# Kernel optimization log

Hardware: AMD Instinct MI355X
Metric: run time of the kernel (lower is better)

The kernel has to match this reference:

```python
import jax, jax.numpy as jnp
import numpy as np

H = 64    # hidden_size
IN = 7    # input_size
Q = 3     # output_size = len(quantiles)
T = 288   # target_len


def _lstm_cell(x, h, c, W_ih, W_hh, b_ih, b_hh):
    # PyTorch gate order: i, f, g, o. W_ih: [4H, in], W_hh: [4H, H]
    gates = x @ W_ih.T + h @ W_hh.T + (b_ih + b_hh)  # [B, 4H]
    i, f, g, o = jnp.split(gates, 4, axis=-1)
    i = jax.nn.sigmoid(i)
    f = jax.nn.sigmoid(f)
    g = jnp.tanh(g)
    o = jax.nn.sigmoid(o)
    c_new = f * c + i * g
    h_new = o * jnp.tanh(c_new)
    return h_new, c_new


def setup_inputs() -> dict:
    key = jax.random.key(0)
    ks = jax.random.split(key, 12)
    B, S = 2048, 512
    scale = 1.0 / np.sqrt(H)  # matches PyTorch uniform(-1/sqrt(H), 1/sqrt(H)) magnitude
    u = lambda k, shape: jax.random.uniform(k, shape, jnp.float32, -scale, scale)
    return {
        "x": jax.random.normal(ks[0], (B, S, IN), dtype=jnp.float32),
        "enc_W_ih": u(ks[1], (4 * H, IN)),
        "enc_W_hh": u(ks[2], (4 * H, H)),
        "enc_b_ih": u(ks[3], (4 * H,)),
        "enc_b_hh": u(ks[4], (4 * H,)),
        "dec_W_ih": u(ks[5], (4 * H, Q)),
        "dec_W_hh": u(ks[6], (4 * H, H)),
        "dec_b_ih": u(ks[7], (4 * H,)),
        "dec_b_hh": u(ks[8], (4 * H,)),
        "out_W": u(ks[9], (Q, H)),
        "out_b": u(ks[10], (Q,)),
    }


def reference(x, enc_W_ih, enc_W_hh, enc_b_ih, enc_b_hh,
              dec_W_ih, dec_W_hh, dec_b_ih, dec_b_hh, out_W, out_b):
    B = x.shape[0]
    # ---- Encoder LSTM over the full sequence; keep only final (h, c) ----
    h0 = jnp.zeros((B, H), dtype=x.dtype)
    c0 = jnp.zeros((B, H), dtype=x.dtype)

    def enc_step(carry, x_t):
        h, c = carry
        h, c = _lstm_cell(x_t, h, c, enc_W_ih, enc_W_hh, enc_b_ih, enc_b_hh)
        return (h, c), None

    (h_enc, c_enc), _ = jax.lax.scan(enc_step, (h0, c0), jnp.swapaxes(x, 0, 1))

    # ---- Decoder: each of the T steps restarts from the FIXED encoder state
    # (the original discards the decoder's returned state), feeding back the
    # previous output. Dropout is identity at inference. ----
    def dec_step(dec_in, _):
        h1, _c1 = _lstm_cell(dec_in, h_enc, c_enc,
                             dec_W_ih, dec_W_hh, dec_b_ih, dec_b_hh)
        out = h1 @ out_W.T + out_b  # [B, Q]
        return out, out

    dec_in0 = jnp.zeros((B, Q), dtype=x.dtype)
    _, outputs = jax.lax.scan(dec_step, dec_in0, None, length=T)  # [T, B, Q]
    return jnp.transpose(outputs, (1, 0, 2))  # [B, T, Q]; out_dict[q] = out[:, :, i]
```

## Files before the change

### kernel.cpp

```cpp
#include <hip/hip_runtime.h>

#define HDIM  64
#define INDIM 7
#define QDIM  3
#define TDEC  288
#define SEQ   512
#define NBT   8
#define CHUNK 32
#define HPAD  68
#define GPAD  264
#define HBST  80
#define PXU   264

typedef __attribute__((ext_vector_type(8))) short bf16x8;
typedef __attribute__((ext_vector_type(4))) float f32x4;

__device__ __forceinline__ float fast_rcp(float x) { return __builtin_amdgcn_rcpf(x); }
__device__ __forceinline__ float sigm(float x) { return fast_rcp(1.0f + __expf(-x)); }
__device__ __forceinline__ float tanh_f(float x) {
    float e = __expf(2.0f * x);
    return fmaf(-2.0f, fast_rcp(1.0f + e), 1.0f);
}
__device__ __forceinline__ short f2bf(float f) {
    union { float f; unsigned u; } v; v.f = f;
    unsigned r = (v.u + 0x7fffu + ((v.u >> 16) & 1u)) >> 16;
    return (short)r;
}
__device__ __forceinline__ float bf2f(short s) {
    union { unsigned u; float f; } v; v.u = ((unsigned)(unsigned short)s) << 16;
    return v.f;
}

__global__ __launch_bounds__(512, 2)
void enc_dec_kernel(const float* __restrict__ x,
                    const float* __restrict__ eWih, const float* __restrict__ eWhh,
                    const float* __restrict__ ebih, const float* __restrict__ ebhh,
                    const float* __restrict__ dWih, const float* __restrict__ dWhh,
                    const float* __restrict__ dbih, const float* __restrict__ dbhh,
                    const float* __restrict__ oW,   const float* __restrict__ obv,
                    float* __restrict__ out)
{
    __shared__ __align__(16) short lds_hh[2][NBT][HBST];
    __shared__ __align__(16) short lds_xbh[2][CHUNK][NBT][8];
    __shared__ __align__(16) short lds_xbl[2][CHUNK][NBT][8];
    __shared__ __align__(16) short lds_xzero[8];
    __shared__ __align__(16) float lds_px[2][4][NBT][PXU];
    __shared__ __align__(16) float lds_hf[NBT][HPAD];
    __shared__ __align__(16) float lds_cf[NBT][HPAD];
    __shared__ __align__(16) float lds_g[NBT][GPAD];

    const int tid  = threadIdx.x;
    const int lane = tid & 63;
    const int wid  = tid >> 6;
    const int b0   = blockIdx.x * NBT;

    const int m    = lane & 15;
    const int g16  = lane >> 4;
    const int b_act = lane & 7;
    const int tsel  = (lane >> 3) & 1;
    const int u_act = wid * 8 + tsel * 4 + g16;

    bf16x8 a_hi[2][2], a_lo[2][2];
#pragma unroll
    for (int tt = 0; tt < 2; ++tt) {
        const int t = 2 * wid + tt;
        const int row = (m & 3) * 64 + 4 * t + (m >> 2);
#pragma unroll
        for (int kt = 0; kt < 2; ++kt) {
            const float* p = eWhh + (size_t)row * HDIM + kt * 32 + g16 * 8;
            f32x4 v0 = *(const f32x4*)p;
            f32x4 v1 = *(const f32x4*)(p + 4);
#pragma unroll
            for (int e = 0; e < 4; ++e) {
                short hi = f2bf(v0[e]);
                a_hi[tt][kt][e] = hi;
                a_lo[tt][kt][e] = f2bf(v0[e] - bf2f(hi));
            }
#pragma unroll
            for (int e = 0; e < 4; ++e) {
                short hi = f2bf(v1[e]);
                a_hi[tt][kt][4 + e] = hi;
                a_lo[tt][kt][4 + e] = f2bf(v1[e] - bf2f(hi));
            }
        }
    }

    bf16x8 axh[2], axl[2];
#pragma unroll
    for (int tt = 0; tt < 2; ++tt) {
        const int t = 2 * wid + tt;
        const int row = (m & 3) * 64 + 4 * t + (m >> 2);
        if (g16 == 0) {
#pragma unroll
            for (int e = 0; e < 8; ++e) {
                float v = (e < 7) ? eWih[row * INDIM + e] : (ebih[row] + ebhh[row]);
                short hi = f2bf(v);
                axh[tt][e] = hi;
                axl[tt][e] = f2bf(v - bf2f(hi));
            }
        } else {
#pragma unroll
            for (int e = 0; e < 8; ++e) { axh[tt][e] = 0; axl[tt][e] = 0; }
        }
    }

    lds_hh[1][wid][lane] = 0;
    if (tid < 8) lds_xzero[tid] = 0;
    float c_reg = 0.0f;

    auto load_x_chunk = [&](int xbuf, int s0) {
        for (int i = tid; i < NBT * CHUNK * 8; i += 512) {
            int b = i >> 8;
            int r = i & 255;
            int ss = r >> 3;
            int k = r & 7;
            float v = (k < 7) ? x[((size_t)(b0 + b) * SEQ + (s0 + ss)) * INDIM + k] : 1.0f;
            short hi = f2bf(v);
            lds_xbh[xbuf][ss][b][k] = hi;
            lds_xbl[xbuf][ss][b][k] = f2bf(v - bf2f(hi));
        }
    };

    auto compute_xw = [&](int j2) {
        const int sbase = 4 * j2;
        const int xbuf  = (sbase >> 5) & 1;
        const int sr0   = sbase & 31;
        const int col16 = lane & 15;
        const int pxb   = j2 & 1;
        bf16x8 bxh[2], bxl[2];
#pragma unroll
        for (int n = 0; n < 2; ++n) {
            const int srow = sr0 + 2 * n + (col16 >> 3);
            const short* ph = (g16 == 0) ? &lds_xbh[xbuf][srow][lane & 7][0] : &lds_xzero[0];
            const short* pl = (g16 == 0) ? &lds_xbl[xbuf][srow][lane & 7][0] : &lds_xzero[0];
            bxh[n] = *(const bf16x8*)ph;
            bxl[n] = *(const bf16x8*)pl;
        }
#pragma unroll
        for (int tt = 0; tt < 2; ++tt) {
#pragma unroll
            for (int n = 0; n < 2; ++n) {
                f32x4 p = {0, 0, 0, 0};
                p = __builtin_amdgcn_mfma_f32_16x16x32_bf16(axh[tt], bxh[n], p, 0, 0, 0);
                p = __builtin_amdgcn_mfma_f32_16x16x32_bf16(axl[tt], bxh[n], p, 0, 0, 0);
                p = __builtin_amdgcn_mfma_f32_16x16x32_bf16(axh[tt], bxl[n], p, 0, 0, 0);
                const int sl = 2 * n + (col16 >> 3);
                const int u  = 4 * (2 * wid + tt) + (lane >> 4);
                *(f32x4*)&lds_px[pxb][sl][lane & 7][u * 4] = p;
            }
        }
    };

    load_x_chunk(0, 0);
    __syncthreads();
    compute_xw(0);
    __syncthreads();

    for (int s = 0; s < SEQ; ++s) {
        const int cs  = s & (CHUNK - 1);
        const int rb  = (s & 1) ^ 1;
        const int wb  = s & 1;

        f32x4 px4 = *(const f32x4*)&lds_px[(s >> 2) & 1][s & 3][b_act][u_act * 4];

        bf16x8 bh[2];
#pragma unroll
        for (int kt = 0; kt < 2; ++kt)
            bh[kt] = *(const bf16x8*)&lds_hh[rb][b_act][kt * 32 + g16 * 8];

        f32x4 acc0 = {0, 0, 0, 0}, acc1 = {0, 0, 0, 0};
#pragma unroll
        for (int kt = 0; kt < 2; ++kt) {
            acc0 = __builtin_amdgcn_mfma_f32_16x16x32_bf16(a_hi[0][kt], bh[kt], acc0, 0, 0, 0);
            acc1 = __builtin_amdgcn_mfma_f32_16x16x32_bf16(a_hi[1][kt], bh[kt], acc1, 0, 0, 0);
            acc0 = __builtin_amdgcn_mfma_f32_16x16x32_bf16(a_lo[0][kt], bh[kt], acc0, 0, 0, 0);
            acc1 = __builtin_amdgcn_mfma_f32_16x16x32_bf16(a_lo[1][kt], bh[kt], acc1, 0, 0, 0);
        }

        float pre[4];
#pragma unroll
        for (int g = 0; g < 4; ++g) pre[g] = tsel ? acc1[g] : acc0[g];

        {
#pragma unroll
            for (int g = 0; g < 4; ++g) pre[g] += px4[g];
            float ig = sigm(pre[0]), fg = sigm(pre[1]), gg = tanh_f(pre[2]), og = sigm(pre[3]);
            c_reg = fg * c_reg + ig * gg;
            float h = og * tanh_f(c_reg);
            lds_hh[wb][b_act][u_act] = f2bf(h);
            if (s + 1 == SEQ) {
                lds_hf[b_act][u_act] = h;
                lds_cf[b_act][u_act] = c_reg;
            }
        }

        if ((s & 3) == 0 && s + 4 < SEQ) compute_xw((s >> 2) + 1);

        if (cs == 0 && s + CHUNK < SEQ) {
            load_x_chunk(((s >> 5) & 1) ^ 1, s + CHUNK);
        }
        __syncthreads();
    }

    {
        const int row = tid & 255;
        const int gh  = tid >> 8;
        float4 dwhh[16];
#pragma unroll
        for (int m4 = 0; m4 < 16; ++m4)
            dwhh[m4] = *reinterpret_cast<const float4*>(&dWhh[row * HDIM + m4 * 4]);
        const float dbias = dbih[row] + dbhh[row];

        float accd[4];
#pragma unroll
        for (int b = 0; b < 4; ++b) accd[b] = dbias;
#pragma unroll
        for (int m4 = 0; m4 < 16; ++m4) {
            const float4 w = dwhh[m4];
            float4 hv[4];
#pragma unroll
            for (int b = 0; b < 4; ++b)
                hv[b] = *reinterpret_cast<const float4*>(&lds_hf[gh * 4 + b][m4 * 4]);
#pragma unroll
            for (int b = 0; b < 4; ++b) accd[b] = fmaf(hv[b].x, w.x, accd[b]);
#pragma unroll
            for (int b = 0; b < 4; ++b) accd[b] = fmaf(hv[b].y, w.y, accd[b]);
#pragma unroll
            for (int b = 0; b < 4; ++b) accd[b] = fmaf(hv[b].z, w.z, accd[b]);
#pragma unroll
            for (int b = 0; b < 4; ++b) accd[b] = fmaf(hv[b].w, w.w, accd[b]);
        }
#pragma unroll
        for (int b = 0; b < 4; ++b) lds_g[gh * 4 + b][row] = accd[b];
    }
    __syncthreads();

    {
        const int b = wid, j = lane;
        const float c_e = lds_cf[b][j];
        const float gb0 = lds_g[b][j];
        const float gb1 = lds_g[b][HDIM + j];
        const float gb2 = lds_g[b][2 * HDIM + j];
        const float gb3 = lds_g[b][3 * HDIM + j];

        const float w00 = dWih[(0 * HDIM + j) * QDIM + 0], w01 = dWih[(0 * HDIM + j) * QDIM + 1], w02 = dWih[(0 * HDIM + j) * QDIM + 2];
        const float w10 = dWih[(1 * HDIM + j) * QDIM + 0], w11 = dWih[(1 * HDIM + j) * QDIM + 1], w12 = dWih[(1 * HDIM + j) * QDIM + 2];
        const float w20 = dWih[(2 * HDIM + j) * QDIM + 0], w21 = dWih[(2 * HDIM + j) * QDIM + 1], w22 = dWih[(2 * HDIM + j) * QDIM + 2];
        const float w30 = dWih[(3 * HDIM + j) * QDIM + 0], w31 = dWih[(3 * HDIM + j) * QDIM + 1], w32 = dWih[(3 * HDIM + j) * QDIM + 2];
        const float ow0 = oW[0 * HDIM + j], ow1 = oW[1 * HDIM + j], ow2 = oW[2 * HDIM + j];
        const float ob0 = obv[0], ob1 = obv[1], ob2 = obv[2];

        float y0 = 0.0f, y1 = 0.0f, y2 = 0.0f;
        float* outp = out + (size_t)(b0 + b) * TDEC * QDIM;

        for (int t = 0; t < TDEC; ++t) {
            float g0 = gb0 + y0 * w00 + y1 * w01 + y2 * w02;
            float g1 = gb1 + y0 * w10 + y1 * w11 + y2 * w12;
            float g2 = gb2 + y0 * w20 + y1 * w21 + y2 * w22;
            float g3 = gb3 + y0 * w30 + y1 * w31 + y2 * w32;
            float ig = sigm(g0), fg = sigm(g1), gg = tanh_f(g2), og = sigm(g3);
            float c = fg * c_e + ig * gg;
            float h = og * tanh_f(c);
            float r0 = h * ow0, r1 = h * ow1, r2 = h * ow2;
#pragma unroll
            for (int d = 1; d < 64; d <<= 1) {
                r0 += __shfl_xor(r0, d);
                r1 += __shfl_xor(r1, d);
                r2 += __shfl_xor(r2, d);
            }
            y0 = r0 + ob0;
            y1 = r1 + ob1;
            y2 = r2 + ob2;
            if (j < QDIM) outp[t * QDIM + j] = (j == 0) ? y0 : (j == 1) ? y1 : y2;
        }
    }
}

extern "C" void kernel_launch(void* const* d_in, const int* in_sizes, int n_in,
                              void* d_out, int out_size, void* d_ws, size_t ws_size,
                              hipStream_t stream) {
    (void)in_sizes; (void)n_in; (void)d_ws; (void)ws_size; (void)out_size;
    const float* x    = (const float*)d_in[0];
    const float* eWih = (const float*)d_in[1];
    const float* eWhh = (const float*)d_in[2];
    const float* ebih = (const float*)d_in[3];
    const float* ebhh = (const float*)d_in[4];
    const float* dWih = (const float*)d_in[5];
    const float* dWhh = (const float*)d_in[6];
    const float* dbih = (const float*)d_in[7];
    const float* dbhh = (const float*)d_in[8];
    const float* oW   = (const float*)d_in[9];
    const float* obv  = (const float*)d_in[10];
    float* out = (float*)d_out;

    const int B = 2048;
    dim3 grid(B / NBT), block(512);
    enc_dec_kernel<<<grid, block, 0, stream>>>(x, eWih, eWhh, ebih, ebhh,
                                               dWih, dWhh, dbih, dbhh, oW, obv, out);
}
```

Measured before the change: 405.0 us.

## Halve batch tile per block to four rows with 256-thread blocks

Measured after the change: 444.3 us. 1.1x slower.

```diff
diff --git a/kernel.cpp b/kernel.cpp
--- a/kernel.cpp
+++ b/kernel.cpp
@@ -5,7 +5,7 @@
 #define QDIM  3
 #define TDEC  288
 #define SEQ   512
-#define NBT   8
+#define NBT   4
 #define CHUNK 32
 #define HPAD  68
 #define GPAD  264
@@ -31,7 +31,7 @@
     return v.f;
 }
 
-__global__ __launch_bounds__(512, 2)
+__global__ __launch_bounds__(256, 2)
 void enc_dec_kernel(const float* __restrict__ x,
                     const float* __restrict__ eWih, const float* __restrict__ eWhh,
                     const float* __restrict__ ebih, const float* __restrict__ ebhh,
@@ -56,14 +56,14 @@
 
     const int m    = lane & 15;
     const int g16  = lane >> 4;
-    const int b_act = lane & 7;
-    const int tsel  = (lane >> 3) & 1;
-    const int u_act = wid * 8 + tsel * 4 + g16;
-
-    bf16x8 a_hi[2][2], a_lo[2][2];
-#pragma unroll
-    for (int tt = 0; tt < 2; ++tt) {
-        const int t = 2 * wid + tt;
+    const int b_act = lane & 3;
+    const int tsel  = (lane >> 2) & 3;
+    const int u_act = wid * 16 + tsel * 4 + g16;
+
+    bf16x8 a_hi[4][2], a_lo[4][2];
+#pragma unroll
+    for (int tt = 0; tt < 4; ++tt) {
+        const int t = 4 * wid + tt;
         const int row = (m & 3) * 64 + 4 * t + (m >> 2);
 #pragma unroll
         for (int kt = 0; kt < 2; ++kt) {
@@ -85,10 +85,10 @@
         }
     }
 
-    bf16x8 axh[2], axl[2];
-#pragma unroll
-    for (int tt = 0; tt < 2; ++tt) {
-        const int t = 2 * wid + tt;
+    bf16x8 axh[4], axl[4];
+#pragma unroll
+    for (int tt = 0; tt < 4; ++tt) {
+        const int t = 4 * wid + tt;
         const int row = (m & 3) * 64 + 4 * t + (m >> 2);
         if (g16 == 0) {
 #pragma unroll
@@ -109,7 +109,7 @@
     float c_reg = 0.0f;
 
     auto load_x_chunk = [&](int xbuf, int s0) {
-        for (int i = tid; i < NBT * CHUNK * 8; i += 512) {
+        for (int i = tid; i < NBT * CHUNK * 8; i += 256) {
             int b = i >> 8;
             int r = i & 255;
             int ss = r >> 3;
@@ -125,29 +125,24 @@
         const int sbase = 4 * j2;
         const int xbuf  = (sbase >> 5) & 1;
         const int sr0   = sbase & 31;
-        const int col16 = lane & 15;
         const int pxb   = j2 & 1;
-        bf16x8 bxh[2], bxl[2];
-#pragma unroll
-        for (int n = 0; n < 2; ++n) {
-            const int srow = sr0 + 2 * n + (col16 >> 3);
-            const short* ph = (g16 == 0) ? &lds_xbh[xbuf][srow][lane & 7][0] : &lds_xzero[0];
-            const short* pl = (g16 == 0) ? &lds_xbl[xbuf][srow][lane & 7][0] : &lds_xzero[0];
-            bxh[n] = *(const bf16x8*)ph;
-            bxl[n] = *(const bf16x8*)pl;
-        }
-#pragma unroll
-        for (int tt = 0; tt < 2; ++tt) {
-#pragma unroll
-            for (int n = 0; n < 2; ++n) {
-                f32x4 p = {0, 0, 0, 0};
-                p = __builtin_amdgcn_mfma_f32_16x16x32_bf16(axh[tt], bxh[n], p, 0, 0, 0);
-                p = __builtin_amdgcn_mfma_f32_16x16x32_bf16(axl[tt], bxh[n], p, 0, 0, 0);
-                p = __builtin_amdgcn_mfma_f32_16x16x32_bf16(axh[tt], bxl[n], p, 0, 0, 0);
-                const int sl = 2 * n + (col16 >> 3);
-                const int u  = 4 * (2 * wid + tt) + (lane >> 4);
-                *(f32x4*)&lds_px[pxb][sl][lane & 7][u * 4] = p;
-            }
+        const int bb    = lane & 3;
+        const int slot  = (lane >> 2) & 3;
+        bf16x8 bxh, bxl;
+        {
+            const short* ph = (g16 == 0) ? &lds_xbh[xbuf][sr0 + slot][bb][0] : &lds_xzero[0];
+            const short* pl = (g16 == 0) ? &lds_xbl[xbuf][sr0 + slot][bb][0] : &lds_xzero[0];
+            bxh = *(const bf16x8*)ph;
+            bxl = *(const bf16x8*)pl;
+        }
+#pragma unroll
+        for (int tt = 0; tt < 4; ++tt) {
+            f32x4 p = {0, 0, 0, 0};
+            p = __builtin_amdgcn_mfma_f32_16x16x32_bf16(axh[tt], bxh, p, 0, 0, 0);
+            p = __builtin_amdgcn_mfma_f32_16x16x32_bf16(axl[tt], bxh, p, 0, 0, 0);
+            p = __builtin_amdgcn_mfma_f32_16x16x32_bf16(axh[tt], bxl, p, 0, 0, 0);
+            const int u = 4 * (4 * wid + tt) + (lane >> 4);
+            *(f32x4*)&lds_px[pxb][slot][bb][u * 4] = p;
         }
     };
 
@@ -168,18 +163,24 @@
         for (int kt = 0; kt < 2; ++kt)
             bh[kt] = *(const bf16x8*)&lds_hh[rb][b_act][kt * 32 + g16 * 8];
 
-        f32x4 acc0 = {0, 0, 0, 0}, acc1 = {0, 0, 0, 0};
+        f32x4 acc[4] = {{0,0,0,0},{0,0,0,0},{0,0,0,0},{0,0,0,0}};
 #pragma unroll
         for (int kt = 0; kt < 2; ++kt) {
-            acc0 = __builtin_amdgcn_mfma_f32_16x16x32_bf16(a_hi[0][kt], bh[kt], acc0, 0, 0, 0);
-            acc1 = __builtin_amdgcn_mfma_f32_16x16x32_bf16(a_hi[1][kt], bh[kt], acc1, 0, 0, 0);
-            acc0 = __builtin_amdgcn_mfma_f32_16x16x32_bf16(a_lo[0][kt], bh[kt], acc0, 0, 0, 0);
-            acc1 = __builtin_amdgcn_mfma_f32_16x16x32_bf16(a_lo[1][kt], bh[kt], acc1, 0, 0, 0);
+#pragma unroll
+            for (int tt = 0; tt < 4; ++tt)
+                acc[tt] = __builtin_amdgcn_mfma_f32_16x16x32_bf16(a_hi[tt][kt], bh[kt], acc[tt], 0, 0, 0);
+#pragma unroll
+            for (int tt = 0; tt < 4; ++tt)
+                acc[tt] = __builtin_amdgcn_mfma_f32_16x16x32_bf16(a_lo[tt][kt], bh[kt], acc[tt], 0, 0, 0);
         }
 
         float pre[4];
 #pragma unroll
-        for (int g = 0; g < 4; ++g) pre[g] = tsel ? acc1[g] : acc0[g];
+        for (int g = 0; g < 4; ++g) {
+            float s01 = (tsel & 1) ? acc[1][g] : acc[0][g];
+            float s23 = (tsel & 1) ? acc[3][g] : acc[2][g];
+            pre[g] = (tsel & 2) ? s23 : s01;
+        }
 
         {
 #pragma unroll
@@ -203,35 +204,34 @@
     }
 
     {
-        const int row = tid & 255;
-        const int gh  = tid >> 8;
+        const int row = wid * HDIM + lane;
         float4 dwhh[16];
 #pragma unroll
         for (int m4 = 0; m4 < 16; ++m4)
             dwhh[m4] = *reinterpret_cast<const float4*>(&dWhh[row * HDIM + m4 * 4]);
         const float dbias = dbih[row] + dbhh[row];
 
-        float accd[4];
-#pragma unroll
-        for (int b = 0; b < 4; ++b) accd[b] = dbias;
+        float accd[NBT];
+#pragma unroll
+        for (int b = 0; b < NBT; ++b) accd[b] = dbias;
 #pragma unroll
         for (int m4 = 0; m4 < 16; ++m4) {
             const float4 w = dwhh[m4];
-            float4 hv[4];
-#pragma unroll
-            for (int b = 0; b < 4; ++b)
-                hv[b] = *reinterpret_cast<const float4*>(&lds_hf[gh * 4 + b][m4 * 4]);
-#pragma unroll
-            for (int b = 0; b < 4; ++b) accd[b] = fmaf(hv[b].x, w.x, accd[b]);
-#pragma unroll
-            for (int b = 0; b < 4; ++b) accd[b] = fmaf(hv[b].y, w.y, accd[b]);
-#pragma unroll
-            for (int b = 0; b < 4; ++b) accd[b] = fmaf(hv[b].z, w.z, accd[b]);
-#pragma unroll
-            for (int b = 0; b < 4; ++b) accd[b] = fmaf(hv[b].w, w.w, accd[b]);
-        }
-#pragma unroll
-        for (int b = 0; b < 4; ++b) lds_g[gh * 4 + b][row] = accd[b];
+            float4 hv[NBT];
+#pragma unroll
+            for (int b = 0; b < NBT; ++b)
+                hv[b] = *reinterpret_cast<const float4*>(&lds_hf[b][m4 * 4]);
+#pragma unroll
+            for (int b = 0; b < NBT; ++b) accd[b] = fmaf(hv[b].x, w.x, accd[b]);
+#pragma unroll
+            for (int b = 0; b < NBT; ++b) accd[b] = fmaf(hv[b].y, w.y, accd[b]);
+#pragma unroll
+            for (int b = 0; b < NBT; ++b) accd[b] = fmaf(hv[b].z, w.z, accd[b]);
+#pragma unroll
+            for (int b = 0; b < NBT; ++b) accd[b] = fmaf(hv[b].w, w.w, accd[b]);
+        }
+#pragma unroll
+        for (int b = 0; b < NBT; ++b) lds_g[b][row] = accd[b];
     }
     __syncthreads();
 
@@ -294,7 +294,7 @@
     float* out = (float*)d_out;
 
     const int B = 2048;
-    dim3 grid(B / NBT), block(512);
+    dim3 grid(B / NBT), block(256);
     enc_dec_kernel<<<grid, block, 0, stream>>>(x, eWih, eWhh, ebih, ebhh,
                                                dWih, dWhh, dbih, dbhh, oW, obv, out);
 }
```

## Drop bf16 hi/lo split for encoder W_hh and use DPP wave reductions

Applied to the files above, without the earlier changes.

Result: faster. 356.0 us, median of 2 (-12.1%).

```diff
diff --git a/kernel.cpp b/kernel.cpp
--- a/kernel.cpp
+++ b/kernel.cpp
@@ -29,6 +29,21 @@
 __device__ __forceinline__ float bf2f(short s) {
     union { unsigned u; float f; } v; v.u = ((unsigned)(unsigned short)s) << 16;
     return v.f;
+}
+
+template<int CTRL>
+__device__ __forceinline__ float dpp_add(float v) {
+    int p = __builtin_amdgcn_update_dpp(0, __float_as_int(v), CTRL, 0xF, 0xF, true);
+    return v + __int_as_float(p);
+}
+__device__ __forceinline__ float wave_sum(float v) {
+    v = dpp_add<0xB1>(v);
+    v = dpp_add<0x4E>(v);
+    v = dpp_add<0x124>(v);
+    v = dpp_add<0x128>(v);
+    v += __shfl_xor(v, 16);
+    v += __shfl_xor(v, 32);
+    return v;
 }
 
 __global__ __launch_bounds__(512, 2)
@@ -60,7 +75,7 @@
     const int tsel  = (lane >> 3) & 1;
     const int u_act = wid * 8 + tsel * 4 + g16;
 
-    bf16x8 a_hi[2][2], a_lo[2][2];
+    bf16x8 a_h[2][2];
 #pragma unroll
     for (int tt = 0; tt < 2; ++tt) {
         const int t = 2 * wid + tt;
@@ -71,17 +86,9 @@
             f32x4 v0 = *(const f32x4*)p;
             f32x4 v1 = *(const f32x4*)(p + 4);
 #pragma unroll
-            for (int e = 0; e < 4; ++e) {
-                short hi = f2bf(v0[e]);
-                a_hi[tt][kt][e] = hi;
-                a_lo[tt][kt][e] = f2bf(v0[e] - bf2f(hi));
-            }
-#pragma unroll
-            for (int e = 0; e < 4; ++e) {
-                short hi = f2bf(v1[e]);
-                a_hi[tt][kt][4 + e] = hi;
-                a_lo[tt][kt][4 + e] = f2bf(v1[e] - bf2f(hi));
-            }
+            for (int e = 0; e < 4; ++e) a_h[tt][kt][e]     = f2bf(v0[e]);
+#pragma unroll
+            for (int e = 0; e < 4; ++e) a_h[tt][kt][4 + e] = f2bf(v1[e]);
         }
     }
 
@@ -171,10 +178,8 @@
         f32x4 acc0 = {0, 0, 0, 0}, acc1 = {0, 0, 0, 0};
 #pragma unroll
         for (int kt = 0; kt < 2; ++kt) {
-            acc0 = __builtin_amdgcn_mfma_f32_16x16x32_bf16(a_hi[0][kt], bh[kt], acc0, 0, 0, 0);
-            acc1 = __builtin_amdgcn_mfma_f32_16x16x32_bf16(a_hi[1][kt], bh[kt], acc1, 0, 0, 0);
-            acc0 = __builtin_amdgcn_mfma_f32_16x16x32_bf16(a_lo[0][kt], bh[kt], acc0, 0, 0, 0);
-            acc1 = __builtin_amdgcn_mfma_f32_16x16x32_bf16(a_lo[1][kt], bh[kt], acc1, 0, 0, 0);
+            acc0 = __builtin_amdgcn_mfma_f32_16x16x32_bf16(a_h[0][kt], bh[kt], acc0, 0, 0, 0);
+            acc1 = __builtin_amdgcn_mfma_f32_16x16x32_bf16(a_h[1][kt], bh[kt], acc1, 0, 0, 0);
         }
 
         float pre[4];
@@ -261,13 +266,9 @@
             float ig = sigm(g0), fg = sigm(g1), gg = tanh_f(g2), og = sigm(g3);
             float c = fg * c_e + ig * gg;
             float h = og * tanh_f(c);
-            float r0 = h * ow0, r1 = h * ow1, r2 = h * ow2;
-#pragma unroll
-            for (int d = 1; d < 64; d <<= 1) {
-                r0 += __shfl_xor(r0, d);
-                r1 += __shfl_xor(r1, d);
-                r2 += __shfl_xor(r2, d);
-            }
+            float r0 = wave_sum(h * ow0);
+            float r1 = wave_sum(h * ow1);
+            float r2 = wave_sum(h * ow2);
             y0 = r0 + ob0;
             y1 = r1 + ob1;
             y2 = r2 + ob2;
```
